# Kernel tuning notes

Hardware: AMD Instinct MI355X
Metric: run time of the kernel (lower is better)

The kernel has to match this reference:

```python
import jax, jax.numpy as jnp
import numpy as np

B, M, D, K = 512, 32, 2048, 3
COUPLING_STRENGTH = 0.1
SPATIAL_DECAY = 2.0


def setup_inputs() -> dict:
    key = jax.random.key(0)
    k1, k2 = jax.random.split(key)
    x = jax.random.normal(k1, (B, M, D), dtype=jnp.float32)  # stacked module activities
    w = jax.random.normal(k2, (D, K), dtype=jnp.float32) * 0.1  # conv1d weight [out=D, in=1, K] squeezed
    return {"x": x, "w": w}


def reference(x, w):
    # x: [B, M, D] stacked module activities; w: [D, K] field-propagation conv weight.
    b, m, d = x.shape
    k = w.shape[1]
    pad = k // 2
    # Conv1d(in=1, out=D, padding=pad) followed by mean over the length dim is
    # exactly: E[b,m,c] = (1/D) * sum_k w[c,k] * S_k, where S_k is the sum of x
    # over the input positions actually touched by tap k (zero padding drops edges).
    T = x.sum(-1)                       # [B, M] total sum
    cs = jnp.cumsum(x, axis=-1)         # [B, M, D] prefix sums
    S_list = []
    for kk in range(k):                 # K is a small static constant
        o = kk - pad                    # tap offset; touched indices [max(0,o), D-1+min(0,o)]
        if o > 0:
            S_list.append(T - cs[..., o - 1])       # drop first o entries
        elif o < 0:
            S_list.append(cs[..., d - 1 + o])       # drop last |o| entries
        else:
            S_list.append(T)
    S = jnp.stack(S_list, axis=-1)      # [B, M, K]
    fields = jnp.einsum('bmk,dk->bmd', S, w) / d  # electric fields [B, M, D]
    # distance-decayed coupling with self-term excluded (i != j in the loop)
    idx = jnp.arange(m)
    decay = jnp.exp(-jnp.abs(idx[:, None] - idx[None, :]).astype(x.dtype) / SPATIAL_DECAY)
    decay = decay * (1.0 - jnp.eye(m, dtype=x.dtype))  # zero diagonal
    weighted = jnp.einsum('ij,bjd->bid', decay, fields)  # [B, M, D]
    return x + COUPLING_STRENGTH * weighted
```

## Files before the change

kernel.cpp:

```cpp
#include <hip/hip_runtime.h>
#include <stdint.h>

#define B_ 512
#define M_ 32
#define D_ 2048

typedef float fvec4 __attribute__((ext_vector_type(4)));

static __device__ __forceinline__ uint32_t pk_bf16(float lo, float hi) {
    uint32_t r;
    asm("v_cvt_pk_bf16_f32 %0, %1, %2" : "=v"(r) : "v"(lo), "v"(hi));
    return r;
}
static __device__ __forceinline__ float bf_lo(uint32_t u) { return __uint_as_float(u << 16); }
static __device__ __forceinline__ float bf_hi(uint32_t u) { return __uint_as_float(u & 0xFFFF0000u); }

__global__ __launch_bounds__(1024) void ephaptic_fused(const float* __restrict__ x,
                                                       const float* __restrict__ w,
                                                       float* __restrict__ out) {
    const int b = blockIdx.x;
    const int tid = threadIdx.x;
    const int m = tid >> 5;
    const int t = tid & 31;

    __shared__ float sT[M_], sF[M_], sL[M_];
    __shared__ fvec4 sC[M_];

    const size_t rowbase = ((size_t)b * M_ + m) * (size_t)D_;
    const fvec4* row = (const fvec4*)(x + rowbase);

    uint32_t u[32];
    float sum = 0.f;
    float first = 0.f, last = 0.f;
#pragma unroll
    for (int q = 0; q < 16; ++q) {
        const fvec4 v = row[t + 32 * q];
        sum += (v.x + v.y) + (v.z + v.w);
        if (q == 0)  first = v.x;
        if (q == 15) last  = v.w;
        u[2 * q]     = pk_bf16(v.x, v.y);
        u[2 * q + 1] = pk_bf16(v.z, v.w);
    }
#pragma unroll
    for (int off = 16; off > 0; off >>= 1)
        sum += __shfl_xor(sum, off, 64);
    if (t == 0)  { sT[m] = sum; sF[m] = first; }
    if (t == 31) { sL[m] = last; }
    __syncthreads();

    if (tid < M_) {
        const int i = tid;
        float r0 = 0.f, r1 = 0.f, r2 = 0.f;
        for (int j = 0; j < M_; ++j) {
            if (j == i) continue;
            const float dij = __expf(-0.5f * fabsf((float)(i - j)));
            const float T = sT[j];
            r0 += dij * (T - sL[j]);
            r1 += dij * T;
            r2 += dij * (T - sF[j]);
        }
        const float s = 0.1f / (float)D_;
        sC[i] = (fvec4){r0 * s, r1 * s, r2 * s, 0.f};
    }
    __syncthreads();

    const fvec4 co = sC[m];
    const fvec4* wf = (const fvec4*)w;
    fvec4* orow = (fvec4*)(out + rowbase);
#pragma unroll
    for (int q = 0; q < 16; ++q) {
        const int c4 = t + 32 * q;
        const fvec4 w0 = wf[c4 * 3 + 0];
        const fvec4 w1 = wf[c4 * 3 + 1];
        const fvec4 w2 = wf[c4 * 3 + 2];
        fvec4 o;
        o.x = bf_lo(u[2 * q])     + co.x * w0.x + co.y * w0.y + co.z * w0.z;
        o.y = bf_hi(u[2 * q])     + co.x * w0.w + co.y * w1.x + co.z * w1.y;
        o.z = bf_lo(u[2 * q + 1]) + co.x * w1.z + co.y * w1.w + co.z * w2.x;
        o.w = bf_hi(u[2 * q + 1]) + co.x * w2.y + co.y * w2.z + co.z * w2.w;
        __builtin_nontemporal_store(o, orow + c4);
    }
}

extern "C" void kernel_launch(void* const* d_in, const int* in_sizes, int n_in,
                              void* d_out, int out_size, void* d_ws, size_t ws_size,
                              hipStream_t stream) {
    const float* x = (const float*)d_in[0];
    const float* w = (const float*)d_in[1];
    float* out = (float*)d_out;
    ephaptic_fused<<<B_, 1024, 0, stream>>>(x, w, out);
}
```

Measured before the change: 55.67 us.

## Re-read x from memory in output pass and hoist per-column weights

Drops the bf16 register cache of x and instead re-reads each x row from global memory in the output pass, expecting the block's x tile to still be cached. The output pass is remapped so each thread owns one column quad across 16 rows. Each thread then loads its three weight vectors once rather than once per row. This lowers register pressure and removes the bf16 rounding of x, making the result exact fp32. The cost is a second read of x that may go to DRAM if the cache has evicted it.

After: 66.32 us. 1.19x slower.

```diff
diff --git a/kernel.cpp b/kernel.cpp
--- a/kernel.cpp
+++ b/kernel.cpp
@@ -7,45 +7,36 @@
 
 typedef float fvec4 __attribute__((ext_vector_type(4)));
 
-static __device__ __forceinline__ uint32_t pk_bf16(float lo, float hi) {
-    uint32_t r;
-    asm("v_cvt_pk_bf16_f32 %0, %1, %2" : "=v"(r) : "v"(lo), "v"(hi));
-    return r;
-}
-static __device__ __forceinline__ float bf_lo(uint32_t u) { return __uint_as_float(u << 16); }
-static __device__ __forceinline__ float bf_hi(uint32_t u) { return __uint_as_float(u & 0xFFFF0000u); }
-
 __global__ __launch_bounds__(1024) void ephaptic_fused(const float* __restrict__ x,
                                                        const float* __restrict__ w,
                                                        float* __restrict__ out) {
     const int b = blockIdx.x;
     const int tid = threadIdx.x;
-    const int m = tid >> 5;
-    const int t = tid & 31;
 
     __shared__ float sT[M_], sF[M_], sL[M_];
     __shared__ fvec4 sC[M_];
 
-    const size_t rowbase = ((size_t)b * M_ + m) * (size_t)D_;
-    const fvec4* row = (const fvec4*)(x + rowbase);
+    const float* xb = x + (size_t)b * M_ * D_;
+    float* ob = out + (size_t)b * M_ * D_;
 
-    uint32_t u[32];
-    float sum = 0.f;
-    float first = 0.f, last = 0.f;
+    {
+        const int m = tid >> 5;
+        const int t = tid & 31;
+        const fvec4* row = (const fvec4*)(xb + (size_t)m * D_);
+        float sum = 0.f, first = 0.f, last = 0.f;
 #pragma unroll
-    for (int q = 0; q < 16; ++q) {
-        const fvec4 v = row[t + 32 * q];
-        sum += (v.x + v.y) + (v.z + v.w);
-        if (q == 0)  first = v.x;
-        if (q == 15) last  = v.w;
-        u[2 * q]     = pk_bf16(v.x, v.y);
-        u[2 * q + 1] = pk_bf16(v.z, v.w);
+        for (int q = 0; q < 16; ++q) {
+            const fvec4 v = row[t + 32 * q];
+            sum += (v.x + v.y) + (v.z + v.w);
+            if (q == 0)  first = v.x;
+            if (q == 15) last  = v.w;
+        }
+#pragma unroll
+        for (int off = 16; off > 0; off >>= 1)
+            sum += __shfl_xor(sum, off, 64);
+        if (t == 0)  { sT[m] = sum; sF[m] = first; }
+        if (t == 31) { sL[m] = last; }
     }
-#pragma unroll
-    for (int off = 16; off > 0; off >>= 1)
-        sum += __shfl_xor(sum, off, 64);
-    if (t == 0)  { sT[m] = sum; sF[m] = first; }
-    if (t == 31) { sL[m] = last; }
     __syncthreads();
 
     if (tid < M_) {
@@ -64,21 +55,25 @@
     }
     __syncthreads();
 
-    const fvec4 co = sC[m];
-    const fvec4* wf = (const fvec4*)w;
-    fvec4* orow = (fvec4*)(out + rowbase);
-#pragma unroll
-    for (int q = 0; q < 16; ++q) {
-        const int c4 = t + 32 * q;
-        const fvec4 w0 = wf[c4 * 3 + 0];
-        const fvec4 w1 = wf[c4 * 3 + 1];
-        const fvec4 w2 = wf[c4 * 3 + 2];
-        fvec4 o;
-        o.x = bf_lo(u[2 * q])     + co.x * w0.x + co.y * w0.y + co.z * w0.z;
-        o.y = bf_hi(u[2 * q])     + co.x * w0.w + co.y * w1.x + co.z * w1.y;
-        o.z = bf_lo(u[2 * q + 1]) + co.x * w1.z + co.y * w1.w + co.z * w2.x;
-        o.w = bf_hi(u[2 * q + 1]) + co.x * w2.y + co.y * w2.z + co.z * w2.w;
-        __builtin_nontemporal_store(o, orow + c4);
+    {
+        const int p = tid & 511;
+        const int h = tid >> 9;
+        const fvec4* wf = (const fvec4*)w;
+        const fvec4 w0 = wf[p * 3 + 0];
+        const fvec4 w1 = wf[p * 3 + 1];
+        const fvec4 w2 = wf[p * 3 + 2];
+#pragma unroll 4
+        for (int r = 0; r < 16; ++r) {
+            const int row = h * 16 + r;
+            const fvec4 c = sC[row];
+            const fvec4 xv = ((const fvec4*)(xb + (size_t)row * D_))[p];
+            fvec4 o;
+            o.x = xv.x + c.x * w0.x + c.y * w0.y + c.z * w0.z;
+            o.y = xv.y + c.x * w0.w + c.y * w1.x + c.z * w1.y;
+            o.z = xv.z + c.x * w1.z + c.y * w1.w + c.z * w2.x;
+            o.w = xv.w + c.x * w2.y + c.y * w2.z + c.z * w2.w;
+            __builtin_nontemporal_store(o, ((fvec4*)(ob + (size_t)row * D_)) + p);
+        }
     }
 }
 
```
